# Optimization experiments

Measured on AMD Instinct MI355X. Metric: run time of the kernel, lower is better.

## Reference

```python
import jax, jax.numpy as jnp
import numpy as np

N = 50000      # nodes
E = 800000     # edges (avg degree 16)
IN = 128       # in_dim
OUT = 128      # out_dim
K = 4          # Chebyshev order
NEIG = 64      # num_eigs
H = 128        # eigval_hidden_dim
BN_EPS = 1e-5


def setup_inputs() -> dict:
    key = jax.random.key(0)
    ks = jax.random.split(key, 12)
    feature = jax.random.normal(ks[0], (N, IN), jnp.float32)
    # linear over concat of (K Chebyshev blocks + 1 spectral block) = (K+1)*IN
    lin_w = jax.random.normal(ks[1], ((K + 1) * IN, OUT), jnp.float32) / np.sqrt((K + 1) * IN)
    lin_b = jnp.zeros((OUT,), jnp.float32)
    # eigval_filter MLP: 1 -> H -> H -> 1 (ReLU between)
    ew0 = jax.random.normal(ks[2], (1, H), jnp.float32)
    eb0 = jnp.zeros((H,), jnp.float32)
    ew1 = jax.random.normal(ks[3], (H, H), jnp.float32) / np.sqrt(H)
    eb1 = jnp.zeros((H,), jnp.float32)
    ew2 = jax.random.normal(ks[4], (H, 1), jnp.float32) / np.sqrt(H)
    eb2 = jnp.zeros((1,), jnp.float32)
    bn_gamma = jnp.ones((OUT,), jnp.float32)
    bn_beta = jnp.zeros((OUT,), jnp.float32)
    lambda_max = jnp.ones((1,), jnp.float32)
    # cached (detached) spectral data for the graph
    evecs = jax.random.normal(ks[5], (N, NEIG), jnp.float32)
    evals = jax.random.uniform(ks[6], (NEIG,), jnp.float32)
    edge_src = jax.random.randint(ks[7], (E,), 0, N, jnp.int32).astype(jnp.int64)
    edge_dst = jax.random.randint(ks[8], (E,), 0, N, jnp.int32).astype(jnp.int64)
    return dict(feature=feature, lin_w=lin_w, lin_b=lin_b, ew0=ew0, eb0=eb0,
                ew1=ew1, eb1=eb1, ew2=ew2, eb2=eb2, bn_gamma=bn_gamma,
                bn_beta=bn_beta, lambda_max=lambda_max, evecs=evecs,
                evals=evals, edge_src=edge_src, edge_dst=edge_dst)


def reference(feature, lin_w, lin_b, ew0, eb0, ew1, eb1, ew2, eb2,
              bn_gamma, bn_beta, lambda_max, evecs, evals, edge_src, edge_dst):
    src = edge_src.astype(jnp.int32)
    dst = edge_dst.astype(jnp.int32)
    # in-degrees (messages arrive at dst) and D^-1/2, clamped at 1
    deg = jax.ops.segment_sum(jnp.ones((E,), jnp.float32), dst, num_segments=N)
    d_sqrt = jnp.clip(deg, 1.0, None) ** -0.5  # [N]
    d_sqrt = d_sqrt[:, None]                   # [N,1]

    def unn_laplacian(x):
        m = (x * d_sqrt)[src]                              # [E,IN]
        agg = jax.ops.segment_sum(m, dst, num_segments=N)  # [N,IN]
        return agg * d_sqrt

    re_norm = 2.0 / lambda_max  # broadcast scalar (per-node in dgl, constant here)

    X0 = feature
    blocks = [X0]
    h = unn_laplacian(X0)
    X1 = -re_norm * h + X0 * (re_norm - 1.0)
    blocks.append(X1)
    for _ in range(2, K):
        h = unn_laplacian(X1)
        Xi = -2.0 * re_norm * h + X1 * 2.0 * (re_norm - 1.0) - X0
        blocks.append(Xi)
        X1, X0 = Xi, X1

    # spectral filtering: evecs^T f, scale by MLP(evals), project back
    z = jax.nn.relu(evals[:, None] @ ew0 + eb0)   # [NEIG,H]
    z = jax.nn.relu(z @ ew1 + eb1)                # [NEIG,H]
    ef = z @ ew2 + eb2                            # [NEIG,1]
    hs = jnp.einsum('ne,nf->ef', evecs, feature)  # [NEIG,IN]
    hs = ef * hs
    hs = jnp.einsum('ne,ef->nf', evecs, hs)       # [N,IN]
    blocks.append(hs)

    Xt = jnp.concatenate(blocks, axis=1)          # [N,(K+1)*IN]
    out = Xt @ lin_w + lin_b                      # [N,OUT]

    # BatchNorm1d (training-mode batch statistics, biased variance)
    mu = jnp.mean(out, axis=0)
    var = jnp.mean((out - mu) ** 2, axis=0)
    out = (out - mu) * jax.lax.rsqrt(var + BN_EPS) * bn_gamma + bn_beta
    out = jax.nn.relu(out)
    # dropout p=0.0 -> identity; residual disabled
    return out
```

## Files before the change

kernel.cpp:

```cpp
#include <hip/hip_runtime.h>

#define N_NODES 50000
#define N_EDGES 800000
#define IN_F    128
#define OUT_F   128
#define NEIG    64
#define HDIM    128
#define BN_EPSF 1e-5f
#define XB_ROWS 50048
#define XB_COLS 640
#define SCAN_BLK 49
#define HSP_BLOCKS 521
#define HSP_NODES 96
#define RED_CHUNK 33
#define N_REP 8
#define RANK_BLOCKS 391

typedef __attribute__((ext_vector_type(8))) short short8;
typedef __attribute__((ext_vector_type(4))) float floatx4;

#define OFF_XB      0
#define OFF_X1F     (XB_ROWS * XB_COLS / 2)
#define OFF_X2F     (OFF_X1F + N_NODES * IN_F)
#define OFF_WT      (OFF_X2F + N_NODES * IN_F)
#define OFF_DSQRT   (OFF_WT + 40960)
#define OFF_HS      (OFF_DSQRT + N_NODES)
#define OFF_EF      (OFF_HS + NEIG * OUT_F)
#define OFF_COLSUM  (OFF_EF + NEIG)
#define OFF_COLSQ   (OFF_COLSUM + OUT_F)
#define OFF_DEG     (OFF_COLSQ + OUT_F)
#define OFF_ROWSTART (OFF_DEG + N_REP * N_NODES)
#define OFF_CSR     (OFF_ROWSTART + N_NODES + 1)
#define OFF_BSUM    (OFF_CSR + N_EDGES)
#define OFF_RANK    (OFF_BSUM + 64)
#define OFF_RS4     (OFF_RANK + N_EDGES)

static __device__ inline unsigned short f2bf(float f) {
    union { float f; unsigned int u; } v; v.f = f;
    unsigned int r = (v.u + 0x7FFFu + ((v.u >> 16) & 1u)) >> 16;
    return (unsigned short)r;
}
static __device__ inline float bf2f(unsigned int u16) {
    union { unsigned int u; float f; } v; v.u = u16 << 16;
    return v.f;
}

__global__ __launch_bounds__(256) void k_prep(const float* __restrict__ feat,
                                              const float* __restrict__ W,
                                              unsigned short* __restrict__ Xb,
                                              unsigned short* __restrict__ Wt,
                                              int* __restrict__ degR,
                                              float* __restrict__ small) {
    int b = blockIdx.x;
    if (b < 3125) {
        int t = b * 256 + threadIdx.x;
        int n = t >> 4, c8 = (t & 15) * 8;
        float4 a = *(const float4*)&feat[n * IN_F + c8];
        float4 bb = *(const float4*)&feat[n * IN_F + c8 + 4];
        ushort4 o0, o1;
        o0.x = f2bf(a.x); o0.y = f2bf(a.y); o0.z = f2bf(a.z); o0.w = f2bf(a.w);
        o1.x = f2bf(bb.x); o1.y = f2bf(bb.y); o1.z = f2bf(bb.z); o1.w = f2bf(bb.w);
        *(ushort4*)&Xb[(size_t)n * XB_COLS + c8]     = o0;
        *(ushort4*)&Xb[(size_t)n * XB_COLS + c8 + 4] = o1;
    } else if (b < 3445) {
        int t = (b - 3125) * 256 + threadIdx.x;
        int k = t >> 7, n = t & 127;
        Wt[n * 640 + k] = f2bf(W[k * 128 + n]);
    } else {
        int i = (b - 3445) * 256 + threadIdx.x;
        if (i < N_REP * N_NODES) degR[i] = 0;
        if (i < NEIG * OUT_F + NEIG + 2 * OUT_F) small[i] = 0.0f;
    }
}

__global__ __launch_bounds__(256) void k_stage2(const float* __restrict__ evecs,
                                                const float* __restrict__ feat,
                                                float* __restrict__ partials,
                                                const float* __restrict__ evals,
                                                const float* __restrict__ ew0,
                                                const float* __restrict__ eb0,
                                                const float* __restrict__ ew1,
                                                const float* __restrict__ eb1,
                                                const float* __restrict__ ew2,
                                                const float* __restrict__ eb2,
                                                float* __restrict__ ef,
                                                int* __restrict__ degR,
                                                const int* __restrict__ dst,
                                                int* __restrict__ rank) {
    int b = blockIdx.x;
    int t = threadIdx.x;
    if (b < HSP_BLOCKS) {
        __shared__ float sEv[32 * NEIG];
        __shared__ float sFt[32 * IN_F];
        int e0 = (t >> 5) * 8;
        int f0 = (t & 31) * 4;
        float acc[8][4];
#pragma unroll
        for (int r = 0; r < 8; ++r)
#pragma unroll
            for (int c = 0; c < 4; ++c) acc[r][c] = 0.0f;

        int n0 = b * HSP_NODES;
        for (int ch = 0; ch < HSP_NODES; ch += 32) {
            int base = n0 + ch;
            {
                int r = t >> 3, c = (t & 7) * 8;
                int n = base + r;
                float4 a, bb;
                if (n < N_NODES) {
                    a = *(const float4*)&evecs[(size_t)n * NEIG + c];
                    bb = *(const float4*)&evecs[(size_t)n * NEIG + c + 4];
                } else {
                    a = make_float4(0, 0, 0, 0); bb = a;
                }
                *(float4*)&sEv[r * NEIG + c] = a;
                *(float4*)&sEv[r * NEIG + c + 4] = bb;
            }
            {
                int r = t >> 3, c = (t & 7) * 16;
                int n = base + r;
#pragma unroll
                for (int q = 0; q < 4; ++q) {
                    float4 v = (n < N_NODES) ? *(const float4*)&feat[(size_t)n * IN_F + c + q * 4]
                                             : make_float4(0, 0, 0, 0);
                    *(float4*)&sFt[r * IN_F + c + q * 4] = v;
                }
            }
            __syncthreads();
#pragma unroll 2
            for (int i = 0; i < 32; ++i) {
                float4 ev0 = *(float4*)&sEv[i * NEIG + e0];
                float4 ev1 = *(float4*)&sEv[i * NEIG + e0 + 4];
                float4 fv  = *(float4*)&sFt[i * IN_F + f0];
                float evv[8] = {ev0.x, ev0.y, ev0.z, ev0.w, ev1.x, ev1.y, ev1.z, ev1.w};
#pragma unroll
                for (int r = 0; r < 8; ++r) {
                    acc[r][0] += evv[r] * fv.x;
                    acc[r][1] += evv[r] * fv.y;
                    acc[r][2] += evv[r] * fv.z;
                    acc[r][3] += evv[r] * fv.w;
                }
            }
            __syncthreads();
        }
        float* p = &partials[(size_t)b * (NEIG * IN_F)];
#pragma unroll
        for (int r = 0; r < 8; ++r)
            *(float4*)&p[(e0 + r) * IN_F + f0] = make_float4(acc[r][0], acc[r][1], acc[r][2], acc[r][3]);
    } else if (b < HSP_BLOCKS + 32) {
        __shared__ float z0[2][HDIM];
        __shared__ float red[2][HDIM];
        int sub = t >> 7, j = t & 127;
        int i = (b - HSP_BLOCKS) * 2 + sub;
        float ev = evals[i];
        z0[sub][j] = fmaxf(0.0f, ev * ew0[j] + eb0[j]);
        __syncthreads();
        float s0 = 0.f, s1 = 0.f, s2 = 0.f, s3 = 0.f;
        for (int h = 0; h < HDIM; h += 4) {
            s0 += z0[sub][h]     * ew1[(h) * HDIM + j];
            s1 += z0[sub][h + 1] * ew1[(h + 1) * HDIM + j];
            s2 += z0[sub][h + 2] * ew1[(h + 2) * HDIM + j];
            s3 += z0[sub][h + 3] * ew1[(h + 3) * HDIM + j];
        }
        float z1 = fmaxf(0.0f, eb1[j] + s0 + s1 + s2 + s3);
        red[sub][j] = z1 * ew2[j];
        __syncthreads();
        for (int off = 64; off > 0; off >>= 1) {
            if (j < off) red[sub][j] += red[sub][j + off];
            __syncthreads();
        }
        if (j == 0) ef[i] = red[sub][0] + eb2[0];
    } else {
        unsigned xcc;
        asm volatile("s_getreg_b32 %0, hwreg(HW_REG_XCC_ID)" : "=s"(xcc));
        int rep = (int)(xcc & (N_REP - 1));
        int* cnt = &degR[rep * N_NODES];
        int bb = b - (HSP_BLOCKS + 32);
        int base = bb * 2048 + t;
        int d[8], rk[8];
#pragma unroll
        for (int k = 0; k < 8; ++k) {
            int e = base + k * 256;
            d[k] = (e < N_EDGES) ? dst[e] : 0;
        }
#pragma unroll
        for (int k = 0; k < 8; ++k) {
            int e = base + k * 256;
            if (e < N_EDGES) rk[k] = atomicAdd(&cnt[d[k]], 1);
        }
#pragma unroll
        for (int k = 0; k < 8; ++k) {
            int e = base + k * 256;
            if (e < N_EDGES) rank[e] = rk[k] | (rep << 24);
        }
    }
}

__global__ __launch_bounds__(1024) void k_stage3(int* __restrict__ degR,
                                                 int* __restrict__ row_start,
                                                 int* __restrict__ bsum,
                                                 const float* __restrict__ partials,
                                                 float* __restrict__ hs_small) {
    int b = blockIdx.x;
    int t = threadIdx.x;
    if (b < SCAN_BLK) {
        __shared__ int sd[1024];
        int i = b * 1024 + t;
        int d0 = 0, d1 = 0, d2 = 0, d3 = 0, d4 = 0, d5 = 0, d6 = 0, d7 = 0;
        if (i < N_NODES) {
            d0 = degR[i];
            d1 = degR[N_NODES + i];
            d2 = degR[2 * N_NODES + i];
            d3 = degR[3 * N_NODES + i];
            d4 = degR[4 * N_NODES + i];
            d5 = degR[5 * N_NODES + i];
            d6 = degR[6 * N_NODES + i];
            d7 = degR[7 * N_NODES + i];
        }
        int total = d0 + d1 + d2 + d3 + d4 + d5 + d6 + d7;
        sd[t] = total;
        __syncthreads();
        for (int off = 1; off < 1024; off <<= 1) {
            int v = (t >= off) ? sd[t - off] : 0;
            __syncthreads();
            sd[t] += v;
            __syncthreads();
        }
        if (i < N_NODES) {
            row_start[i] = sd[t] - total;
            degR[i] = total;
            int p = d0;
            degR[N_NODES + i] = p;     p += d1;
            degR[2 * N_NODES + i] = p; p += d2;
            degR[3 * N_NODES + i] = p; p += d3;
            degR[4 * N_NODES + i] = p; p += d4;
            degR[5 * N_NODES + i] = p; p += d5;
            degR[6 * N_NODES + i] = p; p += d6;
            degR[7 * N_NODES + i] = p;
        }
        if (t == 1023) bsum[b] = sd[1023];
    } else {
        int b2 = b - SCAN_BLK;
        int grp = b2 & 7;
        int chunk = b2 >> 3;
        int idx = grp * 1024 + t;
        int j0 = chunk * RED_CHUNK;
        int j1 = min(j0 + RED_CHUNK, HSP_BLOCKS);
        float s = 0.0f;
        for (int j = j0; j < j1; ++j) s += partials[(size_t)j * (NEIG * IN_F) + idx];
        atomicAdd(&hs_small[idx], s);
    }
}

__global__ __launch_bounds__(1024) void k_scan3(const int* __restrict__ degR,
                                                int* __restrict__ row_start,
                                                const int* __restrict__ bsum,
                                                float* __restrict__ dsq,
                                                int* __restrict__ rs4) {
    __shared__ int sOff;
    int t = threadIdx.x;
    if (t < 64) {
        int orig = (t < SCAN_BLK) ? bsum[t] : 0;
        int v = orig;
        for (int off = 1; off < 64; off <<= 1) {
            int u = __shfl_up(v, off);
            if (t >= off) v += u;
        }
        if (t == blockIdx.x) sOff = v - orig;
    }
    __syncthreads();
    int i = blockIdx.x * 1024 + t;
    if (i < N_NODES) {
        int r = row_start[i] + sOff;
        row_start[i] = r;
        rs4[i] = r;
#pragma unroll
        for (int rep = 1; rep < N_REP; ++rep)
            rs4[rep * N_NODES + i] = r + degR[rep * N_NODES + i];
        dsq[i] = rsqrtf((float)max(degR[i], 1));
    }
    if (i == 0) row_start[N_NODES] = N_EDGES;
}

__global__ __launch_bounds__(256) void k_stage6(const int* __restrict__ src,
                                                const int* __restrict__ dst,
                                                const int* __restrict__ rank,
                                                const int* __restrict__ rs4,
                                                int* __restrict__ csr_src,
                                                unsigned short* __restrict__ Xb,
                                                const float* __restrict__ evecs,
                                                const float* __restrict__ hs_small,
                                                const float* __restrict__ ef) {
    int b = blockIdx.x;
    int t = threadIdx.x;
    if (b < 3125) {
        int e = b * 256 + t;
        if (e < N_EDGES) {
            int rv = rank[e];
            int rep = rv >> 24;
            csr_src[rs4[rep * N_NODES + dst[e]] + (rv & 0xFFFFFF)] = src[e];
        }
    } else {
        __shared__ float sShs[NEIG * HDIM];
        __shared__ float sEv[32 * NEIG];
        int n0 = (b - 3125) * 32;
        {
            float efv = ef[t >> 2];
            int pbase = t * 32;
#pragma unroll
            for (int q = 0; q < 8; ++q) {
                float4 v = *(const float4*)&hs_small[pbase + q * 4];
                v.x *= efv; v.y *= efv; v.z *= efv; v.w *= efv;
                *(float4*)&sShs[pbase + q * 4] = v;
            }
        }
        {
            int r = t >> 3, c = (t & 7) * 8;
            int n = n0 + r;
            float4 a, bb;
            if (n < N_NODES) {
                a = *(const float4*)&evecs[(size_t)n * NEIG + c];
                bb = *(const float4*)&evecs[(size_t)n * NEIG + c + 4];
            } else {
                a = make_float4(0, 0, 0, 0); bb = a;
            }
            *(float4*)&sEv[r * NEIG + c] = a;
            *(float4*)&sEv[r * NEIG + c + 4] = bb;
        }
        __syncthreads();
        int nb = (t >> 5) * 4;
        int f0 = (t & 31) * 4;
        float acc[4][4];
#pragma unroll
        for (int q = 0; q < 4; ++q)
#pragma unroll
            for (int c = 0; c < 4; ++c) acc[q][c] = 0.0f;
        for (int e = 0; e < NEIG; ++e) {
            float4 sv = *(float4*)&sShs[e * HDIM + f0];
#pragma unroll
            for (int q = 0; q < 4; ++q) {
                float evv = sEv[(nb + q) * NEIG + e];
                acc[q][0] += evv * sv.x;
                acc[q][1] += evv * sv.y;
                acc[q][2] += evv * sv.z;
                acc[q][3] += evv * sv.w;
            }
        }
#pragma unroll
        for (int q = 0; q < 4; ++q) {
            int n = n0 + nb + q;
            if (n < N_NODES) {
                ushort4 o;
                o.x = f2bf(acc[q][0]); o.y = f2bf(acc[q][1]);
                o.z = f2bf(acc[q][2]); o.w = f2bf(acc[q][3]);
                *(ushort4*)&Xb[(size_t)n * XB_COLS + 4 * IN_F + f0] = o;
            }
        }
    }
}

__global__ __launch_bounds__(256) void k_gather(const int* __restrict__ row_start,
                                                const int* __restrict__ csr_src,
                                                const float* __restrict__ dsq,
                                                const unsigned short* __restrict__ srcb,
                                                const unsigned short* __restrict__ prevb,
                                                const unsigned short* __restrict__ ppb,
                                                unsigned short* __restrict__ outb,
                                                const float* __restrict__ lm, int first) {
    int n = (blockIdx.x * 256 + threadIdx.x) >> 6;
    int lane = threadIdx.x & 63;
    if (n >= N_NODES) return;
    float rn = 2.0f / lm[0];
    float ax = 0.0f, ay = 0.0f;
    int beg = row_start[n], end = row_start[n + 1];
    int i = beg;
    for (; i + 16 <= end; i += 16) {
        int s[16]; float c[16]; unsigned int p[16];
#pragma unroll
        for (int j = 0; j < 16; ++j) s[j] = __builtin_amdgcn_readfirstlane(csr_src[i + j]);
#pragma unroll
        for (int j = 0; j < 16; ++j) c[j] = dsq[s[j]];
#pragma unroll
        for (int j = 0; j < 16; ++j)
            p[j] = *(const unsigned int*)&srcb[(size_t)s[j] * XB_COLS + lane * 2];
#pragma unroll
        for (int j = 0; j < 16; ++j) {
            ax += c[j] * bf2f(p[j] & 0xffffu);
            ay += c[j] * bf2f(p[j] >> 16);
        }
    }
    for (; i + 8 <= end; i += 8) {
        int s[8]; float c[8]; unsigned int p[8];
#pragma unroll
        for (int j = 0; j < 8; ++j) s[j] = __builtin_amdgcn_readfirstlane(csr_src[i + j]);
#pragma unroll
        for (int j = 0; j < 8; ++j) c[j] = dsq[s[j]];
#pragma unroll
        for (int j = 0; j < 8; ++j)
            p[j] = *(const unsigned int*)&srcb[(size_t)s[j] * XB_COLS + lane * 2];
#pragma unroll
        for (int j = 0; j < 8; ++j) {
            ax += c[j] * bf2f(p[j] & 0xffffu);
            ay += c[j] * bf2f(p[j] >> 16);
        }
    }
    for (; i + 4 <= end; i += 4) {
        int s[4]; float c[4]; unsigned int p[4];
#pragma unroll
        for (int j = 0; j < 4; ++j) s[j] = __builtin_amdgcn_readfirstlane(csr_src[i + j]);
#pragma unroll
        for (int j = 0; j < 4; ++j) c[j] = dsq[s[j]];
#pragma unroll
        for (int j = 0; j < 4; ++j)
            p[j] = *(const unsigned int*)&srcb[(size_t)s[j] * XB_COLS + lane * 2];
#pragma unroll
        for (int j = 0; j < 4; ++j) {
            ax += c[j] * bf2f(p[j] & 0xffffu);
            ay += c[j] * bf2f(p[j] >> 16);
        }
    }
    for (; i < end; ++i) {
        int s = __builtin_amdgcn_readfirstlane(csr_src[i]);
        float sc = dsq[s];
        unsigned int pv = *(const unsigned int*)&srcb[(size_t)s * XB_COLS + lane * 2];
        ax += sc * bf2f(pv & 0xffffu);
        ay += sc * bf2f(pv >> 16);
    }
    float ds = dsq[n];
    float a = (first ? -rn : -2.0f * rn) * ds;
    float b = first ? (rn - 1.0f) : 2.0f * (rn - 1.0f);
    unsigned int pu = *(const unsigned int*)&prevb[(size_t)n * XB_COLS + lane * 2];
    float rx = a * ax + b * bf2f(pu & 0xffffu);
    float ry = a * ay + b * bf2f(pu >> 16);
    if (ppb) {
        unsigned int qu = *(const unsigned int*)&ppb[(size_t)n * XB_COLS + lane * 2];
        rx -= bf2f(qu & 0xffffu);
        ry -= bf2f(qu >> 16);
    }
    unsigned int packed = (unsigned int)f2bf(rx) | ((unsigned int)f2bf(ry) << 16);
    *(unsigned int*)&outb[(size_t)n * XB_COLS + lane * 2] = packed;
}

__global__ __launch_bounds__(256) void k_gemm(const unsigned short* __restrict__ Xb,
                                              const unsigned short* __restrict__ Wt,
                                              const float* __restrict__ bias,
                                              float* __restrict__ out,
                                              float* __restrict__ colsum,
                                              float* __restrict__ colsq) {
    __shared__ unsigned short sA[128 * 32];
    __shared__ unsigned short sB[128 * 32];
    __shared__ float cs[4][OUT_F];
    __shared__ float cq[4][OUT_F];
    int tid = threadIdx.x;
    int wave = tid >> 6, lane = tid & 63;
    int quad = lane >> 4, m16 = lane & 15;
    int row0 = blockIdx.x * 128;

    floatx4 acc[2][8];
#pragma unroll
    for (int mt = 0; mt < 2; ++mt)
#pragma unroll
        for (int nt = 0; nt < 8; ++nt) acc[mt][nt] = (floatx4)(0.0f);

    int r  = tid >> 2;
    int c8 = (tid & 3) * 8;
    int gr0 = min(row0 + r, N_NODES - 1);
    int gr1 = min(row0 + r + 64, N_NODES - 1);

    for (int k0 = 0; k0 < 640; k0 += 32) {
        *(uint4*)&sA[r * 32 + c8]        = *(const uint4*)&Xb[(size_t)gr0 * XB_COLS + k0 + c8];
        *(uint4*)&sA[(r + 64) * 32 + c8] = *(const uint4*)&Xb[(size_t)gr1 * XB_COLS + k0 + c8];
        *(uint4*)&sB[r * 32 + c8]        = *(const uint4*)&Wt[r * 640 + k0 + c8];
        *(uint4*)&sB[(r + 64) * 32 + c8] = *(const uint4*)&Wt[(r + 64) * 640 + k0 + c8];
        __syncthreads();
        short8 a0 = *(short8*)&sA[(wave * 32 + m16) * 32 + quad * 8];
        short8 a1 = *(short8*)&sA[(wave * 32 + 16 + m16) * 32 + quad * 8];
#pragma unroll
        for (int nt = 0; nt < 8; ++nt) {
            short8 b = *(short8*)&sB[(nt * 16 + m16) * 32 + quad * 8];
            acc[0][nt] = __builtin_amdgcn_mfma_f32_16x16x32_bf16(a0, b, acc[0][nt], 0, 0, 0);
            acc[1][nt] = __builtin_amdgcn_mfma_f32_16x16x32_bf16(a1, b, acc[1][nt], 0, 0, 0);
        }
        __syncthreads();
    }
#pragma unroll
    for (int nt = 0; nt < 8; ++nt) {
        int col = nt * 16 + m16;
        float bb = bias[col];
        float sv = 0.0f, sq = 0.0f;
#pragma unroll
        for (int mt = 0; mt < 2; ++mt) {
            int rbase = row0 + wave * 32 + mt * 16 + quad * 4;
#pragma unroll
            for (int reg = 0; reg < 4; ++reg) {
                int row = rbase + reg;
                if (row < N_NODES) {
                    float w = acc[mt][nt][reg] + bb;
                    out[(size_t)row * OUT_F + col] = w;
                    sv += w;
                    sq += w * w;
                }
            }
        }
        sv += __shfl_down(sv, 32); sq += __shfl_down(sq, 32);
        sv += __shfl_down(sv, 16); sq += __shfl_down(sq, 16);
        if (lane < 16) { cs[wave][col] = sv; cq[wave][col] = sq; }
    }
    __syncthreads();
    if (tid < OUT_F) {
        float s = cs[0][tid] + cs[1][tid] + cs[2][tid] + cs[3][tid];
        float q = cq[0][tid] + cq[1][tid] + cq[2][tid] + cq[3][tid];
        atomicAdd(&colsum[tid], s);
        atomicAdd(&colsq[tid], q);
    }
}

__global__ void k_bn_apply(float* __restrict__ out, const float* __restrict__ colsum,
                           const float* __restrict__ colsq, const float* __restrict__ gamma,
                           const float* __restrict__ beta) {
    int t = blockIdx.x * 256 + threadIdx.x;
    int n = t >> 5, c = t & 31;
    float4 v = *(float4*)&out[n * OUT_F + c * 4];
    float4 s = *(const float4*)&colsum[c * 4];
    float4 q = *(const float4*)&colsq[c * 4];
    float4 g = *(const float4*)&gamma[c * 4];
    float4 b = *(const float4*)&beta[c * 4];
    const float invN = 1.0f / (float)N_NODES;
    float mux = s.x * invN, muy = s.y * invN, muz = s.z * invN, muw = s.w * invN;
    float ix = rsqrtf(q.x * invN - mux * mux + BN_EPSF);
    float iy = rsqrtf(q.y * invN - muy * muy + BN_EPSF);
    float iz = rsqrtf(q.z * invN - muz * muz + BN_EPSF);
    float iw = rsqrtf(q.w * invN - muw * muw + BN_EPSF);
    v.x = fmaxf(0.0f, (v.x - mux) * ix * g.x + b.x);
    v.y = fmaxf(0.0f, (v.y - muy) * iy * g.y + b.y);
    v.z = fmaxf(0.0f, (v.z - muz) * iz * g.z + b.z);
    v.w = fmaxf(0.0f, (v.w - muw) * iw * g.w + b.w);
    *(float4*)&out[n * OUT_F + c * 4] = v;
}

extern "C" void kernel_launch(void* const* d_in, const int* in_sizes, int n_in,
                              void* d_out, int out_size, void* d_ws, size_t ws_size,
                              hipStream_t stream) {
    const float* feature    = (const float*)d_in[0];
    const float* lin_w      = (const float*)d_in[1];
    const float* lin_b      = (const float*)d_in[2];
    const float* ew0        = (const float*)d_in[3];
    const float* eb0        = (const float*)d_in[4];
    const float* ew1        = (const float*)d_in[5];
    const float* eb1        = (const float*)d_in[6];
    const float* ew2        = (const float*)d_in[7];
    const float* eb2        = (const float*)d_in[8];
    const float* bn_gamma   = (const float*)d_in[9];
    const float* bn_beta    = (const float*)d_in[10];
    const float* lambda_max = (const float*)d_in[11];
    const float* evecs      = (const float*)d_in[12];
    const float* evals      = (const float*)d_in[13];
    const int*   edge_src   = (const int*)d_in[14];
    const int*   edge_dst   = (const int*)d_in[15];

    float* out = (float*)d_out;
    float* ws  = (float*)d_ws;
    unsigned short* Xb = (unsigned short*)(ws + OFF_XB);
    unsigned short* Wt = (unsigned short*)(ws + OFF_WT);
    float* dsq      = ws + OFF_DSQRT;
    float* hs_small = ws + OFF_HS;
    float* ef       = ws + OFF_EF;
    float* colsum   = ws + OFF_COLSUM;
    float* colsq    = ws + OFF_COLSQ;
    int*   degR     = (int*)(ws + OFF_DEG);
    int*   row_start= (int*)(ws + OFF_ROWSTART);
    int*   csr_src  = (int*)(ws + OFF_CSR);
    int*   bsum     = (int*)(ws + OFF_BSUM);
    int*   rank     = (int*)(ws + OFF_RANK);
    int*   rs4      = (int*)(ws + OFF_RS4);
    float* partials = ws + OFF_X1F;

    k_prep<<<5008, 256, 0, stream>>>(feature, lin_w, Xb, Wt, degR, hs_small);

    k_stage2<<<HSP_BLOCKS + 32 + RANK_BLOCKS, 256, 0, stream>>>(evecs, feature, partials,
                                                                evals, ew0, eb0, ew1, eb1, ew2, eb2,
                                                                ef, degR, edge_dst, rank);

    k_stage3<<<SCAN_BLK + 128, 1024, 0, stream>>>(degR, row_start, bsum, partials, hs_small);
    k_scan3<<<SCAN_BLK, 1024, 0, stream>>>(degR, row_start, bsum, dsq, rs4);

    k_stage6<<<3125 + 1563, 256, 0, stream>>>(edge_src, edge_dst, rank, rs4, csr_src,
                                              Xb, evecs, hs_small, ef);

    const int GBLK = (N_NODES * 64 + 255) / 256;
    k_gather<<<GBLK, 256, 0, stream>>>(row_start, csr_src, dsq,
                                       Xb + 0, Xb + 0, (const unsigned short*)nullptr,
                                       Xb + IN_F, lambda_max, 1);
    k_gather<<<GBLK, 256, 0, stream>>>(row_start, csr_src, dsq,
                                       Xb + IN_F, Xb + IN_F, Xb + 0,
                                       Xb + 2 * IN_F, lambda_max, 0);
    k_gather<<<GBLK, 256, 0, stream>>>(row_start, csr_src, dsq,
                                       Xb + 2 * IN_F, Xb + 2 * IN_F, Xb + IN_F,
                                       Xb + 3 * IN_F, lambda_max, 0);

    k_gemm<<<(N_NODES + 127) / 128, 256, 0, stream>>>(Xb, Wt, lin_b, out, colsum, colsq);
    k_bn_apply<<<(N_NODES * 32) / 256, 256, 0, stream>>>(out, colsum, colsq, bn_gamma, bn_beta);
}
```

Measured before the change: 345.6 us.

## Replace global atomic degree counting with LDS-privatized per-chunk histograms

The in-degree and rank computation for the CSR build previously used global atomics on replicated per-XCC counters. It now uses 64 blocks, each owning one node range and one edge chunk, counting with packed 16-bit shared-memory atomics. Per-chunk counts are written to a 16-way degC array, and the scan and scatter kernels are adapted to use it. This removes global atomic traffic and the separate zeroing pass. In exchange, each block reads its whole 50k-edge chunk, so dst is read four times overall, and parallelism drops to 64 blocks.

Result: slower. 375.6 us (+8.7%).

```diff
diff --git a/kernel.cpp b/kernel.cpp
--- a/kernel.cpp
+++ b/kernel.cpp
@@ -13,8 +13,9 @@
 #define HSP_BLOCKS 521
 #define HSP_NODES 96
 #define RED_CHUNK 33
-#define N_REP 8
-#define RANK_BLOCKS 391
+#define N_CHK 16
+#define N_RNG 4
+#define RANKB (N_RNG * N_CHK)
 
 typedef __attribute__((ext_vector_type(8))) short short8;
 typedef __attribute__((ext_vector_type(4))) float floatx4;
@@ -22,6 +23,8 @@
 #define OFF_XB      0
 #define OFF_X1F     (XB_ROWS * XB_COLS / 2)
 #define OFF_X2F     (OFF_X1F + N_NODES * IN_F)
+#define OFF_DEGC    OFF_X2F
+#define OFF_RSC     (OFF_X2F + N_CHK * N_NODES)
 #define OFF_WT      (OFF_X2F + N_NODES * IN_F)
 #define OFF_DSQRT   (OFF_WT + 40960)
 #define OFF_HS      (OFF_DSQRT + N_NODES)
@@ -29,11 +32,10 @@
 #define OFF_COLSUM  (OFF_EF + NEIG)
 #define OFF_COLSQ   (OFF_COLSUM + OUT_F)
 #define OFF_DEG     (OFF_COLSQ + OUT_F)
-#define OFF_ROWSTART (OFF_DEG + N_REP * N_NODES)
+#define OFF_ROWSTART (OFF_DEG + 8 * N_NODES)
 #define OFF_CSR     (OFF_ROWSTART + N_NODES + 1)
 #define OFF_BSUM    (OFF_CSR + N_EDGES)
 #define OFF_RANK    (OFF_BSUM + 64)
-#define OFF_RS4     (OFF_RANK + N_EDGES)
 
 static __device__ inline unsigned short f2bf(float f) {
     union { float f; unsigned int u; } v; v.f = f;
@@ -49,7 +51,6 @@
                                               const float* __restrict__ W,
                                               unsigned short* __restrict__ Xb,
                                               unsigned short* __restrict__ Wt,
-                                              int* __restrict__ degR,
                                               float* __restrict__ small) {
     int b = blockIdx.x;
     if (b < 3125) {
@@ -68,7 +69,6 @@
         Wt[n * 640 + k] = f2bf(W[k * 128 + n]);
     } else {
         int i = (b - 3445) * 256 + threadIdx.x;
-        if (i < N_REP * N_NODES) degR[i] = 0;
         if (i < NEIG * OUT_F + NEIG + 2 * OUT_F) small[i] = 0.0f;
     }
 }
@@ -84,7 +84,7 @@
                                                 const float* __restrict__ ew2,
                                                 const float* __restrict__ eb2,
                                                 float* __restrict__ ef,
-                                                int* __restrict__ degR,
+                                                int* __restrict__ degC,
                                                 const int* __restrict__ dst,
                                                 int* __restrict__ rank) {
     int b = blockIdx.x;
@@ -171,32 +171,35 @@
         }
         if (j == 0) ef[i] = red[sub][0] + eb2[0];
     } else {
-        unsigned xcc;
-        asm volatile("s_getreg_b32 %0, hwreg(HW_REG_XCC_ID)" : "=s"(xcc));
-        int rep = (int)(xcc & (N_REP - 1));
-        int* cnt = &degR[rep * N_NODES];
-        int bb = b - (HSP_BLOCKS + 32);
-        int base = bb * 2048 + t;
-        int d[8], rk[8];
-#pragma unroll
-        for (int k = 0; k < 8; ++k) {
-            int e = base + k * 256;
-            d[k] = (e < N_EDGES) ? dst[e] : 0;
-        }
-#pragma unroll
-        for (int k = 0; k < 8; ++k) {
-            int e = base + k * 256;
-            if (e < N_EDGES) rk[k] = atomicAdd(&cnt[d[k]], 1);
-        }
-#pragma unroll
-        for (int k = 0; k < 8; ++k) {
-            int e = base + k * 256;
-            if (e < N_EDGES) rank[e] = rk[k] | (rep << 24);
-        }
-    }
-}
-
-__global__ __launch_bounds__(1024) void k_stage3(int* __restrict__ degR,
+        __shared__ unsigned int cnt[6250];
+        int rb = b - (HSP_BLOCKS + 32);
+        int g = rb >> 4, c = rb & (N_CHK - 1);
+        for (int k = t; k < 6250; k += 256) cnt[k] = 0;
+        __syncthreads();
+        int nlo = g * 12500;
+        int ebase = c * 50000;
+        for (int off = t; off < 50000; off += 256) {
+            int e = ebase + off;
+            int d = dst[e];
+            int l = d - nlo;
+            if ((unsigned)l < 12500u) {
+                unsigned sh = (l & 1) * 16;
+                unsigned old = atomicAdd(&cnt[l >> 1], 1u << sh);
+                int lrank = (old >> sh) & 0xFFFF;
+                rank[e] = lrank | (c << 24);
+            }
+        }
+        __syncthreads();
+        for (int k = t; k < 6250; k += 256) {
+            unsigned v = cnt[k];
+            int n0 = nlo + k * 2;
+            degC[(size_t)c * N_NODES + n0]     = (int)(v & 0xFFFF);
+            degC[(size_t)c * N_NODES + n0 + 1] = (int)(v >> 16);
+        }
+    }
+}
+
+__global__ __launch_bounds__(1024) void k_stage3(int* __restrict__ degC,
                                                  int* __restrict__ row_start,
                                                  int* __restrict__ bsum,
                                                  const float* __restrict__ partials,
@@ -206,18 +209,13 @@
     if (b < SCAN_BLK) {
         __shared__ int sd[1024];
         int i = b * 1024 + t;
-        int d0 = 0, d1 = 0, d2 = 0, d3 = 0, d4 = 0, d5 = 0, d6 = 0, d7 = 0;
-        if (i < N_NODES) {
-            d0 = degR[i];
-            d1 = degR[N_NODES + i];
-            d2 = degR[2 * N_NODES + i];
-            d3 = degR[3 * N_NODES + i];
-            d4 = degR[4 * N_NODES + i];
-            d5 = degR[5 * N_NODES + i];
-            d6 = degR[6 * N_NODES + i];
-            d7 = degR[7 * N_NODES + i];
-        }
-        int total = d0 + d1 + d2 + d3 + d4 + d5 + d6 + d7;
+        int d[N_CHK];
+#pragma unroll
+        for (int cc = 0; cc < N_CHK; ++cc)
+            d[cc] = (i < N_NODES) ? degC[(size_t)cc * N_NODES + i] : 0;
+        int total = 0;
+#pragma unroll
+        for (int cc = 0; cc < N_CHK; ++cc) total += d[cc];
         sd[t] = total;
         __syncthreads();
         for (int off = 1; off < 1024; off <<= 1) {
@@ -228,15 +226,13 @@
         }
         if (i < N_NODES) {
             row_start[i] = sd[t] - total;
-            degR[i] = total;
-            int p = d0;
-            degR[N_NODES + i] = p;     p += d1;
-            degR[2 * N_NODES + i] = p; p += d2;
-            degR[3 * N_NODES + i] = p; p += d3;
-            degR[4 * N_NODES + i] = p; p += d4;
-            degR[5 * N_NODES + i] = p; p += d5;
-            degR[6 * N_NODES + i] = p; p += d6;
-            degR[7 * N_NODES + i] = p;
+            degC[i] = total;
+            int p = d[0];
+#pragma unroll
+            for (int cc = 1; cc < N_CHK; ++cc) {
+                degC[(size_t)cc * N_NODES + i] = p;
+                p += d[cc];
+            }
         }
         if (t == 1023) bsum[b] = sd[1023];
     } else {
@@ -252,11 +248,11 @@
     }
 }
 
-__global__ __launch_bounds__(1024) void k_scan3(const int* __restrict__ degR,
+__global__ __launch_bounds__(1024) void k_scan3(const int* __restrict__ degC,
                                                 int* __restrict__ row_start,
                                                 const int* __restrict__ bsum,
                                                 float* __restrict__ dsq,
-                                                int* __restrict__ rs4) {
+                                                int* __restrict__ rsC) {
     __shared__ int sOff;
     int t = threadIdx.x;
     if (t < 64) {
@@ -273,11 +269,11 @@
     if (i < N_NODES) {
         int r = row_start[i] + sOff;
         row_start[i] = r;
-        rs4[i] = r;
-#pragma unroll
-        for (int rep = 1; rep < N_REP; ++rep)
-            rs4[rep * N_NODES + i] = r + degR[rep * N_NODES + i];
-        dsq[i] = rsqrtf((float)max(degR[i], 1));
+        rsC[i] = r;
+#pragma unroll
+        for (int cc = 1; cc < N_CHK; ++cc)
+            rsC[(size_t)cc * N_NODES + i] = r + degC[(size_t)cc * N_NODES + i];
+        dsq[i] = rsqrtf((float)max(degC[i], 1));
     }
     if (i == 0) row_start[N_NODES] = N_EDGES;
 }
@@ -285,7 +281,7 @@
 __global__ __launch_bounds__(256) void k_stage6(const int* __restrict__ src,
                                                 const int* __restrict__ dst,
                                                 const int* __restrict__ rank,
-                                                const int* __restrict__ rs4,
+                                                const int* __restrict__ rsC,
                                                 int* __restrict__ csr_src,
                                                 unsigned short* __restrict__ Xb,
                                                 const float* __restrict__ evecs,
@@ -297,8 +293,8 @@
         int e = b * 256 + t;
         if (e < N_EDGES) {
             int rv = rank[e];
-            int rep = rv >> 24;
-            csr_src[rs4[rep * N_NODES + dst[e]] + (rv & 0xFFFFFF)] = src[e];
+            int c = rv >> 24;
+            csr_src[rsC[(size_t)c * N_NODES + dst[e]] + (rv & 0xFFFFFF)] = src[e];
         }
     } else {
         __shared__ float sShs[NEIG * HDIM];
@@ -567,24 +563,24 @@
     float* ef       = ws + OFF_EF;
     float* colsum   = ws + OFF_COLSUM;
     float* colsq    = ws + OFF_COLSQ;
-    int*   degR     = (int*)(ws + OFF_DEG);
+    int*   degC     = (int*)(ws + OFF_DEGC);
+    int*   rsC      = (int*)(ws + OFF_RSC);
     int*   row_start= (int*)(ws + OFF_ROWSTART);
     int*   csr_src  = (int*)(ws + OFF_CSR);
     int*   bsum     = (int*)(ws + OFF_BSUM);
     int*   rank     = (int*)(ws + OFF_RANK);
-    int*   rs4      = (int*)(ws + OFF_RS4);
     float* partials = ws + OFF_X1F;
 
-    k_prep<<<5008, 256, 0, stream>>>(feature, lin_w, Xb, Wt, degR, hs_small);
-
-    k_stage2<<<HSP_BLOCKS + 32 + RANK_BLOCKS, 256, 0, stream>>>(evecs, feature, partials,
-                                                                evals, ew0, eb0, ew1, eb1, ew2, eb2,
-                                                                ef, degR, edge_dst, rank);
-
-    k_stage3<<<SCAN_BLK + 128, 1024, 0, stream>>>(degR, row_start, bsum, partials, hs_small);
-    k_scan3<<<SCAN_BLK, 1024, 0, stream>>>(degR, row_start, bsum, dsq, rs4);
-
-    k_stage6<<<3125 + 1563, 256, 0, stream>>>(edge_src, edge_dst, rank, rs4, csr_src,
+    k_prep<<<3479, 256, 0, stream>>>(feature, lin_w, Xb, Wt, hs_small);
+
+    k_stage2<<<HSP_BLOCKS + 32 + RANKB, 256, 0, stream>>>(evecs, feature, partials,
+                                                          evals, ew0, eb0, ew1, eb1, ew2, eb2,
+                                                          ef, degC, edge_dst, rank);
+
+    k_stage3<<<SCAN_BLK + 128, 1024, 0, stream>>>(degC, row_start, bsum, partials, hs_small);
+    k_scan3<<<SCAN_BLK, 1024, 0, stream>>>(degC, row_start, bsum, dsq, rsC);
+
+    k_stage6<<<3125 + 1563, 256, 0, stream>>>(edge_src, edge_dst, rank, rsC, csr_src,
                                               Xb, evecs, hs_small, ef);
 
     const int GBLK = (N_NODES * 64 + 255) / 256;
```
